# Kernel optimization log

Measured on AMD Instinct MI355X. Metric: run time of the kernel, lower is better.

## Reference

```python
import jax, jax.numpy as jnp
import numpy as np

N = 100000
NFEAT, NHID, NOUT = 512, 256, 64
NUM_LAYERS = 8
ALPHA = 0.1


def setup_inputs() -> dict:
    key = jax.random.key(0)
    ks = jax.random.split(key, 8)
    E = 3200000
    x = jax.random.normal(ks[0], (N, NFEAT), dtype=jnp.float32)
    edge_index = jax.random.randint(ks[1], (2, E), 0, N, dtype=jnp.int64)
    s1 = 1.0 / np.sqrt(NFEAT)
    s2 = 1.0 / np.sqrt(NHID)
    W1 = jax.random.uniform(ks[2], (NFEAT, NHID), jnp.float32, -s1, s1)
    b1 = jax.random.uniform(ks[3], (NHID,), jnp.float32, -s1, s1)
    W2 = jax.random.uniform(ks[4], (NHID, NOUT), jnp.float32, -s2, s2)
    b2 = jax.random.uniform(ks[5], (NOUT,), jnp.float32, -s2, s2)
    # GCN2Conv weight1 per layer (glorot-ish init), shared_weights=True -> single weight
    conv_w = jax.random.normal(ks[6], (NUM_LAYERS, NHID, NHID), dtype=jnp.float32) * s2
    return {"x": x, "edge_index": edge_index, "W1": W1, "b1": b1,
            "W2": W2, "b2": b2, "conv_w": conv_w}


def _gcn_norm(edge_index, num_nodes):
    # add self loops + symmetric normalization D^{-1/2} (A+I) D^{-1/2}
    loops = jnp.arange(num_nodes, dtype=edge_index.dtype)
    row = jnp.concatenate([edge_index[0], loops])
    col = jnp.concatenate([edge_index[1], loops])
    w = jnp.ones(row.shape[0], dtype=jnp.float32)
    deg = jax.ops.segment_sum(w, row, num_segments=num_nodes)
    dinv = jnp.where(deg > 0, jax.lax.rsqrt(deg), 0.0)
    w = dinv[row] * w * dinv[col]
    return row, col, w


def _spmm(row, col, w, x):
    # out[r] += w_e * x[c]   (adj_t @ x)
    return jax.ops.segment_sum(w[:, None] * x[col], row, num_segments=x.shape[0])


def reference(x, edge_index, W1, b1, W2, b2, conv_w):
    row, col, w = _gcn_norm(edge_index, N)
    h = jax.nn.relu(x @ W1 + b1)  # dropout is identity in eval mode
    x0 = h
    for i in range(NUM_LAYERS):
        agg = _spmm(row, col, w, h)
        # GCN2Conv with theta=None -> beta=1: out = ((1-a)*agg + a*x0) @ W
        mixed = (1.0 - ALPHA) * agg + ALPHA * x0
        h = jax.nn.relu(mixed @ conv_w[i] + h)
    return jax.nn.relu(h @ W2 + b2)
```

## Files before the change

### kernel.cpp

```cpp
#include <hip/hip_runtime.h>
#include <hip/hip_bf16.h>

#define NFEAT 512
#define NHID  256
#define NOUT  64
#define NUM_LAYERS 8


__global__ void hist_kernel(const int* __restrict__ ei, int E, int* __restrict__ cnt) {
    int e = blockIdx.x * blockDim.x + threadIdx.x;
    if (e < E) atomicAdd(&cnt[ei[e]], 1);
}

__global__ void dinv_kernel(const int* __restrict__ cnt, float* __restrict__ dinv, int n) {
    int i = blockIdx.x * blockDim.x + threadIdx.x;
    if (i < n) dinv[i] = rsqrtf((float)cnt[i] + 1.0f);
}

__global__ __launch_bounds__(256)
void scan_blocks(const int* __restrict__ cnt, int* __restrict__ out,
                 int* __restrict__ partials, int n) {
    __shared__ int sdata[256];
    int tid  = threadIdx.x;
    int base = blockIdx.x * 1024 + tid * 4;
    int v[4];
    int s = 0;
    #pragma unroll
    for (int j = 0; j < 4; ++j) {
        int x = (base + j < n) ? cnt[base + j] : 0;
        s += x;
        v[j] = s;
    }
    sdata[tid] = s;
    __syncthreads();
    #pragma unroll
    for (int off = 1; off < 256; off <<= 1) {
        int t = (tid >= off) ? sdata[tid - off] : 0;
        __syncthreads();
        sdata[tid] += t;
        __syncthreads();
    }
    int excl = sdata[tid] - s;
    #pragma unroll
    for (int j = 0; j < 4; ++j)
        if (base + j < n) out[base + j] = excl + v[j];
    if (tid == 255) partials[blockIdx.x] = sdata[255];
}

__global__ __launch_bounds__(256)
void scan_partials(int* __restrict__ partials, int nb) {
    __shared__ int sdata[256];
    int tid = threadIdx.x;
    int s = (tid < nb) ? partials[tid] : 0;
    sdata[tid] = s;
    __syncthreads();
    #pragma unroll
    for (int off = 1; off < 256; off <<= 1) {
        int t = (tid >= off) ? sdata[tid - off] : 0;
        __syncthreads();
        sdata[tid] += t;
        __syncthreads();
    }
    if (tid < nb) partials[tid] = sdata[tid] - s;
}

__global__ void scan_add(int* __restrict__ rowptr, const int* __restrict__ partials, int n) {
    int i = blockIdx.x * blockDim.x + threadIdx.x;
    if (i == 0) rowptr[0] = 0;
    if (i < n) rowptr[i + 1] += partials[i >> 10];
}

__global__ void scatter_kernel(const int* __restrict__ ei, int E,
                               const int* __restrict__ rowptr, int* __restrict__ fill,
                               const float* __restrict__ dinv,
                               int* __restrict__ csr_col, float* __restrict__ csr_w) {
    int e = blockIdx.x * blockDim.x + threadIdx.x;
    if (e >= E) return;
    int r = ei[e];
    int c = ei[E + e];
    int pos = rowptr[r] + atomicAdd(&fill[r], 1);
    csr_col[pos] = c;
    csr_w[pos]   = dinv[r] * dinv[c];
}


__global__ __launch_bounds__(256)
void spmm_kernel(const int* __restrict__ rowptr, const int* __restrict__ csr_col,
                 const float* __restrict__ csr_w, const float* __restrict__ dinv,
                 const float* __restrict__ h, const float* __restrict__ x0,
                 float* __restrict__ mixed, int n) {
    int row = blockIdx.x * 4 + (threadIdx.x >> 6);
    if (row >= n) return;
    int lane = threadIdx.x & 63;
    const float4* hv = (const float4*)h;
    float dr = dinv[row];

    float4 v = hv[(size_t)row * 64 + lane];
    float ws = dr * dr;
    float4 acc;
    acc.x = ws * v.x; acc.y = ws * v.y; acc.z = ws * v.z; acc.w = ws * v.w;

    int beg = rowptr[row], end = rowptr[row + 1];
    int j = beg;
    for (; j + 3 < end; j += 4) {
        int c0 = __builtin_amdgcn_readfirstlane(csr_col[j + 0]);
        int c1 = __builtin_amdgcn_readfirstlane(csr_col[j + 1]);
        int c2 = __builtin_amdgcn_readfirstlane(csr_col[j + 2]);
        int c3 = __builtin_amdgcn_readfirstlane(csr_col[j + 3]);
        float w0 = csr_w[j + 0], w1 = csr_w[j + 1];
        float w2 = csr_w[j + 2], w3 = csr_w[j + 3];
        float4 u0 = hv[(size_t)c0 * 64 + lane];
        float4 u1 = hv[(size_t)c1 * 64 + lane];
        float4 u2 = hv[(size_t)c2 * 64 + lane];
        float4 u3 = hv[(size_t)c3 * 64 + lane];
        acc.x += w0 * u0.x; acc.y += w0 * u0.y; acc.z += w0 * u0.z; acc.w += w0 * u0.w;
        acc.x += w1 * u1.x; acc.y += w1 * u1.y; acc.z += w1 * u1.z; acc.w += w1 * u1.w;
        acc.x += w2 * u2.x; acc.y += w2 * u2.y; acc.z += w2 * u2.z; acc.w += w2 * u2.w;
        acc.x += w3 * u3.x; acc.y += w3 * u3.y; acc.z += w3 * u3.z; acc.w += w3 * u3.w;
    }
    for (; j < end; ++j) {
        int   c  = __builtin_amdgcn_readfirstlane(csr_col[j]);
        float wc = csr_w[j];
        float4 u = hv[(size_t)c * 64 + lane];
        acc.x += wc * u.x; acc.y += wc * u.y; acc.z += wc * u.z; acc.w += wc * u.w;
    }
    float4 xv = ((const float4*)x0)[(size_t)row * 64 + lane];
    float4 o;
    o.x = 0.9f * acc.x + 0.1f * xv.x;
    o.y = 0.9f * acc.y + 0.1f * xv.y;
    o.z = 0.9f * acc.z + 0.1f * xv.z;
    o.w = 0.9f * acc.w + 0.1f * xv.w;
    ((float4*)mixed)[(size_t)row * 64 + lane] = o;
}


template <bool RELU>
__global__ __launch_bounds__(256)
void gemm_kernel(const float* __restrict__ A, const float* __restrict__ W,
                 const float* __restrict__ bias, const float* __restrict__ addend,
                 float* __restrict__ out, float* __restrict__ out2,
                 int M, int K, int Nn) {
    __shared__ float As[16][128];
    __shared__ float Bs[16][128];
    int tid = threadIdx.x;
    int bm = blockIdx.x * 128;
    int bn = blockIdx.y * 128;

    int arow = tid >> 1;
    int acol = (tid & 1) * 8;
    int brow = tid >> 4;
    int bcol = (tid & 15) * 8;
    int x = tid & 15, y = tid >> 4;

    float acc[8][8] = {};

    for (int k0 = 0; k0 < K; k0 += 16) {
        {
            int gr = bm + arow;
            float4 v0 = {0,0,0,0}, v1 = {0,0,0,0};
            if (gr < M) {
                const float* p = A + (size_t)gr * K + k0 + acol;
                v0 = *(const float4*)p;
                v1 = *(const float4*)(p + 4);
            }
            As[acol + 0][arow] = v0.x; As[acol + 1][arow] = v0.y;
            As[acol + 2][arow] = v0.z; As[acol + 3][arow] = v0.w;
            As[acol + 4][arow] = v1.x; As[acol + 5][arow] = v1.y;
            As[acol + 6][arow] = v1.z; As[acol + 7][arow] = v1.w;
        }
        {
            float4 v0 = {0,0,0,0}, v1 = {0,0,0,0};
            if (bn + bcol < Nn) {
                const float* p = W + (size_t)(k0 + brow) * Nn + bn + bcol;
                v0 = *(const float4*)p;
                v1 = *(const float4*)(p + 4);
            }
            *(float4*)&Bs[brow][bcol]     = v0;
            *(float4*)&Bs[brow][bcol + 4] = v1;
        }
        __syncthreads();
        #pragma unroll
        for (int k = 0; k < 16; ++k) {
            float a[8], b[8];
            *(float4*)&a[0] = *(const float4*)&As[k][y * 8];
            *(float4*)&a[4] = *(const float4*)&As[k][y * 8 + 4];
            *(float4*)&b[0] = *(const float4*)&Bs[k][x * 8];
            *(float4*)&b[4] = *(const float4*)&Bs[k][x * 8 + 4];
            #pragma unroll
            for (int i = 0; i < 8; ++i)
                #pragma unroll
                for (int j = 0; j < 8; ++j)
                    acc[i][j] = fmaf(a[i], b[j], acc[i][j]);
        }
        __syncthreads();
    }

    #pragma unroll
    for (int i = 0; i < 8; ++i) {
        int gr = bm + y * 8 + i;
        if (gr >= M) continue;
        size_t ro = (size_t)gr * Nn;
        #pragma unroll
        for (int jj = 0; jj < 8; jj += 4) {
            int gc = bn + x * 8 + jj;
            if (gc >= Nn) continue;
            float4 v;
            v.x = acc[i][jj + 0]; v.y = acc[i][jj + 1];
            v.z = acc[i][jj + 2]; v.w = acc[i][jj + 3];
            if (bias) {
                float4 bv = *(const float4*)(bias + gc);
                v.x += bv.x; v.y += bv.y; v.z += bv.z; v.w += bv.w;
            }
            if (addend) {
                float4 ad = *(const float4*)(addend + ro + gc);
                v.x += ad.x; v.y += ad.y; v.z += ad.z; v.w += ad.w;
            }
            if (RELU) {
                v.x = fmaxf(v.x, 0.f); v.y = fmaxf(v.y, 0.f);
                v.z = fmaxf(v.z, 0.f); v.w = fmaxf(v.w, 0.f);
            }
            *(float4*)(out + ro + gc) = v;
            if (out2) *(float4*)(out2 + ro + gc) = v;
        }
    }
}


extern "C" void kernel_launch(void* const* d_in, const int* in_sizes, int n_in,
                              void* d_out, int out_size, void* d_ws, size_t ws_size,
                              hipStream_t stream) {
    const float* x      = (const float*)d_in[0];
    const int*   ei     = (const int*)d_in[1];
    const float* W1     = (const float*)d_in[2];
    const float* b1     = (const float*)d_in[3];
    const float* W2     = (const float*)d_in[4];
    const float* b2     = (const float*)d_in[5];
    const float* conv_w = (const float*)d_in[6];

    const int M = in_sizes[0] / NFEAT;
    const int E = in_sizes[1] / 2;

    char* ws = (char*)d_ws;
    size_t off = 0;
    auto alloc = [&](size_t bytes) -> void* {
        off = (off + 255) & ~(size_t)255;
        void* p = ws + off;
        off += bytes;
        return p;
    };
    int*   cnt      = (int*)  alloc((size_t)M * 4);
    int*   fill     = (int*)  alloc((size_t)M * 4);
    int*   rowptr   = (int*)  alloc((size_t)(M + 1) * 4);
    int*   partials = (int*)  alloc(256 * 4);
    float* dinv     = (float*)alloc((size_t)M * 4);
    int*   csr      = (int*)  alloc((size_t)E * 4);
    float* csr_w    = (float*)alloc((size_t)E * 4);
    float* h        = (float*)alloc((size_t)M * NHID * 4);
    float* x0       = (float*)alloc((size_t)M * NHID * 4);
    float* mixed    = (float*)alloc((size_t)M * NHID * 4);

    if (off > ws_size) return;

    hipMemsetAsync(cnt,  0, (size_t)M * 4, stream);
    hipMemsetAsync(fill, 0, (size_t)M * 4, stream);

    hist_kernel<<<(E + 255) / 256, 256, 0, stream>>>(ei, E, cnt);
    dinv_kernel<<<(M + 255) / 256, 256, 0, stream>>>(cnt, dinv, M);

    int nchunks = (M + 1023) / 1024;
    scan_blocks<<<nchunks, 256, 0, stream>>>(cnt, rowptr + 1, partials, M);
    scan_partials<<<1, 256, 0, stream>>>(partials, nchunks);
    scan_add<<<(M + 255) / 256, 256, 0, stream>>>(rowptr, partials, M);
    scatter_kernel<<<(E + 255) / 256, 256, 0, stream>>>(ei, E, rowptr, fill, dinv,
                                                        csr, csr_w);

    dim3 g1((M + 127) / 128, (NHID + 127) / 128);
    gemm_kernel<true><<<g1, 256, 0, stream>>>(x, W1, b1, nullptr, h, x0, M, NFEAT, NHID);

    for (int l = 0; l < NUM_LAYERS; ++l) {
        spmm_kernel<<<(M + 3) / 4, 256, 0, stream>>>(rowptr, csr, csr_w, dinv, h, x0,
                                                     mixed, M);
        gemm_kernel<true><<<g1, 256, 0, stream>>>(mixed, conv_w + (size_t)l * NHID * NHID,
                                                  nullptr, h, h, nullptr, M, NHID, NHID);
    }

    dim3 g2((M + 127) / 128, 1);
    gemm_kernel<true><<<g2, 256, 0, stream>>>(h, W2, b2, nullptr, (float*)d_out, nullptr,
                                              M, NHID, NOUT);
}
```

Measured before the change: 6.223 ms.

## Split SpMM into two feature-half passes to shrink gather working set

The aggregation kernel now processes only half of the 256 feature columns per launch (float2 per lane at an offset), and is launched twice per layer for the two halves. The intent is to halve the gathered bytes per pass so the working set of h (about 51 MB per half) fits better in the last-level cache, improving hit rates for random neighbor gathers. The cost is reading CSR indices and weights twice, twice the launches, and narrower 8-byte loads per lane.

```diff
diff --git a/kernel.cpp b/kernel.cpp
--- a/kernel.cpp
+++ b/kernel.cpp
@@ -88,17 +88,18 @@
 void spmm_kernel(const int* __restrict__ rowptr, const int* __restrict__ csr_col,
                  const float* __restrict__ csr_w, const float* __restrict__ dinv,
                  const float* __restrict__ h, const float* __restrict__ x0,
-                 float* __restrict__ mixed, int n) {
+                 float* __restrict__ mixed, int n, int f2off) {
     int row = blockIdx.x * 4 + (threadIdx.x >> 6);
     if (row >= n) return;
     int lane = threadIdx.x & 63;
-    const float4* hv = (const float4*)h;
+    const float2* hv = (const float2*)h;
+    size_t fi = (size_t)row * 128 + f2off + lane;
     float dr = dinv[row];
 
-    float4 v = hv[(size_t)row * 64 + lane];
+    float2 v = hv[fi];
     float ws = dr * dr;
-    float4 acc;
-    acc.x = ws * v.x; acc.y = ws * v.y; acc.z = ws * v.z; acc.w = ws * v.w;
+    float2 acc;
+    acc.x = ws * v.x; acc.y = ws * v.y;
 
     int beg = rowptr[row], end = rowptr[row + 1];
     int j = beg;
@@ -109,28 +110,26 @@
         int c3 = __builtin_amdgcn_readfirstlane(csr_col[j + 3]);
         float w0 = csr_w[j + 0], w1 = csr_w[j + 1];
         float w2 = csr_w[j + 2], w3 = csr_w[j + 3];
-        float4 u0 = hv[(size_t)c0 * 64 + lane];
-        float4 u1 = hv[(size_t)c1 * 64 + lane];
-        float4 u2 = hv[(size_t)c2 * 64 + lane];
-        float4 u3 = hv[(size_t)c3 * 64 + lane];
-        acc.x += w0 * u0.x; acc.y += w0 * u0.y; acc.z += w0 * u0.z; acc.w += w0 * u0.w;
-        acc.x += w1 * u1.x; acc.y += w1 * u1.y; acc.z += w1 * u1.z; acc.w += w1 * u1.w;
-        acc.x += w2 * u2.x; acc.y += w2 * u2.y; acc.z += w2 * u2.z; acc.w += w2 * u2.w;
-        acc.x += w3 * u3.x; acc.y += w3 * u3.y; acc.z += w3 * u3.z; acc.w += w3 * u3.w;
+        float2 u0 = hv[(size_t)c0 * 128 + f2off + lane];
+        float2 u1 = hv[(size_t)c1 * 128 + f2off + lane];
+        float2 u2 = hv[(size_t)c2 * 128 + f2off + lane];
+        float2 u3 = hv[(size_t)c3 * 128 + f2off + lane];
+        acc.x += w0 * u0.x; acc.y += w0 * u0.y;
+        acc.x += w1 * u1.x; acc.y += w1 * u1.y;
+        acc.x += w2 * u2.x; acc.y += w2 * u2.y;
+        acc.x += w3 * u3.x; acc.y += w3 * u3.y;
     }
     for (; j < end; ++j) {
         int   c  = __builtin_amdgcn_readfirstlane(csr_col[j]);
         float wc = csr_w[j];
-        float4 u = hv[(size_t)c * 64 + lane];
-        acc.x += wc * u.x; acc.y += wc * u.y; acc.z += wc * u.z; acc.w += wc * u.w;
-    }
-    float4 xv = ((const float4*)x0)[(size_t)row * 64 + lane];
-    float4 o;
+        float2 u = hv[(size_t)c * 128 + f2off + lane];
+        acc.x += wc * u.x; acc.y += wc * u.y;
+    }
+    float2 xv = ((const float2*)x0)[fi];
+    float2 o;
     o.x = 0.9f * acc.x + 0.1f * xv.x;
     o.y = 0.9f * acc.y + 0.1f * xv.y;
-    o.z = 0.9f * acc.z + 0.1f * xv.z;
-    o.w = 0.9f * acc.w + 0.1f * xv.w;
-    ((float4*)mixed)[(size_t)row * 64 + lane] = o;
+    ((float2*)mixed)[fi] = o;
 }
 
 
@@ -277,9 +276,12 @@
     dim3 g1((M + 127) / 128, (NHID + 127) / 128);
     gemm_kernel<true><<<g1, 256, 0, stream>>>(x, W1, b1, nullptr, h, x0, M, NFEAT, NHID);
 
+    int sgrid = (M + 3) / 4;
     for (int l = 0; l < NUM_LAYERS; ++l) {
-        spmm_kernel<<<(M + 3) / 4, 256, 0, stream>>>(rowptr, csr, csr_w, dinv, h, x0,
-                                                     mixed, M);
+        spmm_kernel<<<sgrid, 256, 0, stream>>>(rowptr, csr, csr_w, dinv, h, x0,
+                                               mixed, M, 0);
+        spmm_kernel<<<sgrid, 256, 0, stream>>>(rowptr, csr, csr_w, dinv, h, x0,
+                                               mixed, M, 64);
         gemm_kernel<true><<<g1, 256, 0, stream>>>(mixed, conv_w + (size_t)l * NHID * NHID,
                                                   nullptr, h, h, nullptr, M, NHID, NHID);
     }
```

After: 6.069 ms. -2.5%, faster.

## Bucket CSR neighbors by column chunk and remap GEMM B-tile reads

Applied to the files above, without the earlier changes.

Builds the CSR with each row's neighbors grouped into four column-range bins, using a finer histogram and scan, so gathered neighbor rows come from nearby address ranges and may hit cache better. Setup scratch buffers are now aliased into the mixed buffer, and degrees are derived from the binned rowptr. Separately, the GEMM pads its LDS tiles to 132 and changes each thread's column mapping to two 4-wide groups 64 apart, aimed at reducing LDS bank conflicts and giving more coalesced stores. The bin ordering only changes the order of accumulation within a row.

```diff
diff --git a/kernel.cpp b/kernel.cpp
--- a/kernel.cpp
+++ b/kernel.cpp
@@ -5,16 +5,26 @@
 #define NHID  256
 #define NOUT  64
 #define NUM_LAYERS 8
-
-
-__global__ void hist_kernel(const int* __restrict__ ei, int E, int* __restrict__ cnt) {
+#define CH    4
+
+
+__global__ void hist_kernel(const int* __restrict__ ei, int E, int M,
+                            int* __restrict__ cnt) {
     int e = blockIdx.x * blockDim.x + threadIdx.x;
-    if (e < E) atomicAdd(&cnt[ei[e]], 1);
-}
-
-__global__ void dinv_kernel(const int* __restrict__ cnt, float* __restrict__ dinv, int n) {
+    if (e >= E) return;
+    int r = ei[e];
+    int c = ei[E + e];
+    int chunk = (c * CH) / M;
+    atomicAdd(&cnt[r * CH + chunk], 1);
+}
+
+__global__ void dinv_kernel(const int* __restrict__ rowptr2, float* __restrict__ dinv,
+                            int n) {
     int i = blockIdx.x * blockDim.x + threadIdx.x;
-    if (i < n) dinv[i] = rsqrtf((float)cnt[i] + 1.0f);
+    if (i < n) {
+        int deg = rowptr2[i * CH + CH] - rowptr2[i * CH];
+        dinv[i] = rsqrtf((float)deg + 1.0f);
+    }
 }
 
 __global__ __launch_bounds__(256)
@@ -22,11 +32,11 @@
                  int* __restrict__ partials, int n) {
     __shared__ int sdata[256];
     int tid  = threadIdx.x;
-    int base = blockIdx.x * 1024 + tid * 4;
-    int v[4];
+    int base = blockIdx.x * 4096 + tid * 16;
+    int v[16];
     int s = 0;
     #pragma unroll
-    for (int j = 0; j < 4; ++j) {
+    for (int j = 0; j < 16; ++j) {
         int x = (base + j < n) ? cnt[base + j] : 0;
         s += x;
         v[j] = s;
@@ -42,7 +52,7 @@
     }
     int excl = sdata[tid] - s;
     #pragma unroll
-    for (int j = 0; j < 4; ++j)
+    for (int j = 0; j < 16; ++j)
         if (base + j < n) out[base + j] = excl + v[j];
     if (tid == 255) partials[blockIdx.x] = sdata[255];
 }
@@ -67,25 +77,27 @@
 __global__ void scan_add(int* __restrict__ rowptr, const int* __restrict__ partials, int n) {
     int i = blockIdx.x * blockDim.x + threadIdx.x;
     if (i == 0) rowptr[0] = 0;
-    if (i < n) rowptr[i + 1] += partials[i >> 10];
-}
-
-__global__ void scatter_kernel(const int* __restrict__ ei, int E,
-                               const int* __restrict__ rowptr, int* __restrict__ fill,
+    if (i < n) rowptr[i + 1] += partials[i >> 12];
+}
+
+__global__ void scatter_kernel(const int* __restrict__ ei, int E, int M,
+                               const int* __restrict__ rowptr2, int* __restrict__ fill,
                                const float* __restrict__ dinv,
                                int* __restrict__ csr_col, float* __restrict__ csr_w) {
     int e = blockIdx.x * blockDim.x + threadIdx.x;
     if (e >= E) return;
     int r = ei[e];
     int c = ei[E + e];
-    int pos = rowptr[r] + atomicAdd(&fill[r], 1);
+    int chunk = (c * CH) / M;
+    int bin = r * CH + chunk;
+    int pos = rowptr2[bin] + atomicAdd(&fill[bin], 1);
     csr_col[pos] = c;
     csr_w[pos]   = dinv[r] * dinv[c];
 }
 
 
 __global__ __launch_bounds__(256)
-void spmm_kernel(const int* __restrict__ rowptr, const int* __restrict__ csr_col,
+void spmm_kernel(const int* __restrict__ rowptr2, const int* __restrict__ csr_col,
                  const float* __restrict__ csr_w, const float* __restrict__ dinv,
                  const float* __restrict__ h, const float* __restrict__ x0,
                  float* __restrict__ mixed, int n) {
@@ -100,7 +112,7 @@
     float4 acc;
     acc.x = ws * v.x; acc.y = ws * v.y; acc.z = ws * v.z; acc.w = ws * v.w;
 
-    int beg = rowptr[row], end = rowptr[row + 1];
+    int beg = rowptr2[row * CH], end = rowptr2[row * CH + CH];
     int j = beg;
     for (; j + 3 < end; j += 4) {
         int c0 = __builtin_amdgcn_readfirstlane(csr_col[j + 0]);
@@ -134,14 +146,16 @@
 }
 
 
+#define LDSP 132
+
 template <bool RELU>
 __global__ __launch_bounds__(256)
 void gemm_kernel(const float* __restrict__ A, const float* __restrict__ W,
                  const float* __restrict__ bias, const float* __restrict__ addend,
                  float* __restrict__ out, float* __restrict__ out2,
                  int M, int K, int Nn) {
-    __shared__ float As[16][128];
-    __shared__ float Bs[16][128];
+    __shared__ float As[16][LDSP];
+    __shared__ float Bs[16][LDSP];
     int tid = threadIdx.x;
     int bm = blockIdx.x * 128;
     int bn = blockIdx.y * 128;
@@ -184,8 +198,8 @@
             float a[8], b[8];
             *(float4*)&a[0] = *(const float4*)&As[k][y * 8];
             *(float4*)&a[4] = *(const float4*)&As[k][y * 8 + 4];
-            *(float4*)&b[0] = *(const float4*)&Bs[k][x * 8];
-            *(float4*)&b[4] = *(const float4*)&Bs[k][x * 8 + 4];
+            *(float4*)&b[0] = *(const float4*)&Bs[k][x * 4];
+            *(float4*)&b[4] = *(const float4*)&Bs[k][64 + x * 4];
             #pragma unroll
             for (int i = 0; i < 8; ++i)
                 #pragma unroll
@@ -202,7 +216,7 @@
         size_t ro = (size_t)gr * Nn;
         #pragma unroll
         for (int jj = 0; jj < 8; jj += 4) {
-            int gc = bn + x * 8 + jj;
+            int gc = bn + (jj ? 64 : 0) + x * 4;
             if (gc >= Nn) continue;
             float4 v;
             v.x = acc[i][jj + 0]; v.y = acc[i][jj + 1];
@@ -239,6 +253,7 @@
 
     const int M = in_sizes[0] / NFEAT;
     const int E = in_sizes[1] / 2;
+    const int n2 = M * CH;
 
     char* ws = (char*)d_ws;
     size_t off = 0;
@@ -248,38 +263,39 @@
         off += bytes;
         return p;
     };
-    int*   cnt      = (int*)  alloc((size_t)M * 4);
-    int*   fill     = (int*)  alloc((size_t)M * 4);
-    int*   rowptr   = (int*)  alloc((size_t)(M + 1) * 4);
-    int*   partials = (int*)  alloc(256 * 4);
-    float* dinv     = (float*)alloc((size_t)M * 4);
-    int*   csr      = (int*)  alloc((size_t)E * 4);
-    float* csr_w    = (float*)alloc((size_t)E * 4);
-    float* h        = (float*)alloc((size_t)M * NHID * 4);
-    float* x0       = (float*)alloc((size_t)M * NHID * 4);
-    float* mixed    = (float*)alloc((size_t)M * NHID * 4);
+    int*   rowptr2 = (int*)  alloc((size_t)(n2 + 1) * 4);
+    float* dinv    = (float*)alloc((size_t)M * 4);
+    int*   csr     = (int*)  alloc((size_t)E * 4);
+    float* csr_w   = (float*)alloc((size_t)E * 4);
+    float* h       = (float*)alloc((size_t)M * NHID * 4);
+    float* x0      = (float*)alloc((size_t)M * NHID * 4);
+    float* mixed   = (float*)alloc((size_t)M * NHID * 4);
+
+    int* cnt      = (int*)mixed;
+    int* fill     = (int*)mixed + n2;
+    int* partials = (int*)mixed + 2 * n2;
 
     if (off > ws_size) return;
 
-    hipMemsetAsync(cnt,  0, (size_t)M * 4, stream);
-    hipMemsetAsync(fill, 0, (size_t)M * 4, stream);
-
-    hist_kernel<<<(E + 255) / 256, 256, 0, stream>>>(ei, E, cnt);
-    dinv_kernel<<<(M + 255) / 256, 256, 0, stream>>>(cnt, dinv, M);
-
-    int nchunks = (M + 1023) / 1024;
-    scan_blocks<<<nchunks, 256, 0, stream>>>(cnt, rowptr + 1, partials, M);
-    scan_partials<<<1, 256, 0, stream>>>(partials, nchunks);
-    scan_add<<<(M + 255) / 256, 256, 0, stream>>>(rowptr, partials, M);
-    scatter_kernel<<<(E + 255) / 256, 256, 0, stream>>>(ei, E, rowptr, fill, dinv,
+    hipMemsetAsync(cnt, 0, (size_t)n2 * 2 * 4, stream);
+
+    hist_kernel<<<(E + 255) / 256, 256, 0, stream>>>(ei, E, M, cnt);
+
+    int nblocks = (n2 + 4095) / 4096;
+    scan_blocks<<<nblocks, 256, 0, stream>>>(cnt, rowptr2 + 1, partials, n2);
+    scan_partials<<<1, 256, 0, stream>>>(partials, nblocks);
+    scan_add<<<(n2 + 255) / 256, 256, 0, stream>>>(rowptr2, partials, n2);
+    dinv_kernel<<<(M + 255) / 256, 256, 0, stream>>>(rowptr2, dinv, M);
+    scatter_kernel<<<(E + 255) / 256, 256, 0, stream>>>(ei, E, M, rowptr2, fill, dinv,
                                                         csr, csr_w);
 
     dim3 g1((M + 127) / 128, (NHID + 127) / 128);
     gemm_kernel<true><<<g1, 256, 0, stream>>>(x, W1, b1, nullptr, h, x0, M, NFEAT, NHID);
 
+    int sgrid = (M + 3) / 4;
     for (int l = 0; l < NUM_LAYERS; ++l) {
-        spmm_kernel<<<(M + 3) / 4, 256, 0, stream>>>(rowptr, csr, csr_w, dinv, h, x0,
-                                                     mixed, M);
+        spmm_kernel<<<sgrid, 256, 0, stream>>>(rowptr2, csr, csr_w, dinv, h, x0,
+                                               mixed, M);
         gemm_kernel<true><<<g1, 256, 0, stream>>>(mixed, conv_w + (size_t)l * NHID * NHID,
                                                   nullptr, h, h, nullptr, M, NHID, NHID);
     }
```

New measurement: 6.126 ms. No clear change (-1.6%).
